# Kernel tuning notes

Measured on AMD Instinct MI355X. Metric: run time of the kernel, lower is better.

The kernel has to match this reference:

```python
import jax, jax.numpy as jnp
import numpy as np

B, S, H = 1, 2048, 2048
E, I = 16, 1408
I_SHARED = 5632
TOP_K = 2


def setup_inputs() -> dict:
    key = jax.random.key(0)
    ks = jax.random.split(key, 8)
    scale = 0.02
    return {
        "hidden_states": jax.random.normal(ks[0], (B, S, H), dtype=jnp.float32),
        "router_w": jax.random.normal(ks[1], (H, E), dtype=jnp.float32) * scale,
        "expert_gate_up_w": jax.random.normal(ks[2], (E, H, 2 * I), dtype=jnp.float32) * scale,
        "expert_out_w": jax.random.normal(ks[3], (E, I, H), dtype=jnp.float32) * scale,
        "shared_ffw_gate_w": jax.random.normal(ks[4], (H, I_SHARED), dtype=jnp.float32) * scale,
        "shared_ffw_inter_w": jax.random.normal(ks[5], (H, I_SHARED), dtype=jnp.float32) * scale,
        "shared_ffw_out_w": jax.random.normal(ks[6], (I_SHARED, H), dtype=jnp.float32) * scale,
        "shared_gate_w": jax.random.normal(ks[7], (H, 1), dtype=jnp.float32) * scale,
        "top_k": TOP_K,
    }


def reference(hidden_states, router_w, expert_gate_up_w, expert_out_w,
              shared_ffw_gate_w, shared_ffw_inter_w, shared_ffw_out_w,
              shared_gate_w, top_k):
    b, s, h = hidden_states.shape
    e = router_w.shape[-1]
    x = hidden_states.reshape(-1, h)  # [T, H]

    # --- Router: softmax over experts, top-k, renormalize (norm_top_k_prob=True) ---
    router_logits = x @ router_w                        # [T, E]
    router_probs = jax.nn.softmax(router_logits, -1)
    top_p, top_i = jax.lax.top_k(router_probs, top_k)   # [T, K]
    top_p = top_p / jnp.sum(top_p, axis=-1, keepdims=True)
    # dense routing matrix [E, T] (matches one_hot-sum-transpose in source)
    one_hot = jax.nn.one_hot(top_i, e, dtype=top_p.dtype)  # [T, K, E]
    routing_full = jnp.sum(one_hot * top_p[..., None], axis=1).T  # [E, T]

    # --- Dense per-expert SwiGLU over ALL tokens (as in QwenMoeExperts) ---
    gate_up = jnp.einsum('th,ehm->etm', x, expert_gate_up_w)  # [E, T, 2I]
    gate, up = jnp.split(gate_up, 2, axis=-1)
    hidden = up * jax.nn.silu(gate)                           # [E, T, I]
    expert_out = jnp.einsum('eti,eih->eth', hidden, expert_out_w)  # [E, T, H]
    expert_contribution = jnp.einsum('eth,et->th', expert_out, routing_full)

    # --- Shared expert (SwiGLU MLP) with sigmoid gate ---
    sgate = jax.nn.silu(x @ shared_ffw_gate_w)
    sinter = x @ shared_ffw_inter_w
    shared_out = (sinter * sgate) @ shared_ffw_out_w          # [T, H]
    shared_out = shared_out * jax.nn.sigmoid(x @ shared_gate_w)

    out = (expert_contribution + shared_out).reshape(b, s, h)
    return out, router_logits
```

## Files before the change

kernel.cpp:

```cpp
#include <hip/hip_runtime.h>
#include <math.h>

typedef __attribute__((ext_vector_type(4))) float f32x4;
typedef __attribute__((ext_vector_type(2))) unsigned int u32x2;
typedef __attribute__((ext_vector_type(4))) unsigned int u32x4;
typedef __attribute__((ext_vector_type(8))) unsigned short u16x8;
typedef __attribute__((ext_vector_type(8))) __bf16 bf16x8;
typedef unsigned short ushort_t;

#define H_DIM 2048
#define T_TOK 2048
#define NEXP 16
#define I_DIM 1408
#define I2_DIM 2816
#define IS_DIM 5632
#define MAXROWS 8192

static __device__ __forceinline__ unsigned short f2bf(float f){
  union { float f; unsigned u; } v; v.f = f;
  unsigned r = v.u + 0x7FFFu + ((v.u >> 16) & 1u);
  return (unsigned short)(r >> 16);
}
static __device__ __forceinline__ float bf2f(unsigned short h){
  union { unsigned u; float f; } v; v.u = ((unsigned)h) << 16;
  return v.f;
}
static __device__ __forceinline__ float silu_f(float x){ return x / (1.f + __expf(-x)); }

static __device__ __forceinline__ void gld16(const ushort_t* g, ushort_t* l){
  __builtin_amdgcn_global_load_lds(
      (const __attribute__((address_space(1))) unsigned int*)g,
      (__attribute__((address_space(3))) unsigned int*)l, 16, 0, 0);
}

__global__ void cast_bf16_k(const float* __restrict__ in, ushort_t* __restrict__ out){
  long i = ((long)blockIdx.x * 256 + threadIdx.x) * 8;
  f32x4 a = *(const f32x4*)&in[i];
  f32x4 b = *(const f32x4*)&in[i + 4];
  union { ushort_t s[8]; u32x4 v; } pk;
  #pragma unroll
  for (int j = 0; j < 4; j++){ pk.s[j] = f2bf(a[j]); pk.s[j+4] = f2bf(b[j]); }
  *(u32x4*)&out[i] = pk.v;
}

__global__ void transpose_cast_k(const float* __restrict__ in, ushort_t* __restrict__ out,
                                 int K, int N){
  long zo = (long)blockIdx.z * K * N;
  in += zo; out += zo;
  __shared__ float tl[64][65];
  int n0 = blockIdx.x * 64, k0 = blockIdx.y * 64;
  int tid = threadIdx.x;
  int lr = tid >> 2;
  int lv = (tid & 3) * 4;
  #pragma unroll
  for (int j = 0; j < 4; j++){
    int col = lv + j * 16;
    f32x4 v = *(const f32x4*)&in[(long)(k0 + lr) * N + n0 + col];
    tl[lr][col + 0] = v[0]; tl[lr][col + 1] = v[1];
    tl[lr][col + 2] = v[2]; tl[lr][col + 3] = v[3];
  }
  __syncthreads();
  int nl = tid >> 3;
  int kc = (tid & 7) * 8;
  #pragma unroll
  for (int it = 0; it < 2; it++){
    int n = nl + it * 32;
    union { ushort_t s[8]; u32x4 v; } pk;
    #pragma unroll
    for (int j = 0; j < 8; j++) pk.s[j] = f2bf(tl[kc + j][n]);
    *(u32x4*)&out[(long)(n0 + n) * K + k0 + kc] = pk.v;
  }
}

__global__ void router_k(const float* __restrict__ x, const float* __restrict__ rw,
                         const float* __restrict__ sgw, float* __restrict__ logits,
                         int* __restrict__ counts, int* __restrict__ lists,
                         float* __restrict__ probs, float* __restrict__ sgmul){
  int wid = threadIdx.x >> 6, lane = threadIdx.x & 63;
  int t = blockIdx.x * 4 + wid;
  const float* xr = x + (long)t * H_DIM;
  float acc[17];
  #pragma unroll
  for (int e = 0; e < 17; e++) acc[e] = 0.f;
  for (int h0 = lane * 4; h0 < H_DIM; h0 += 256){
    f32x4 xv = *(const f32x4*)&xr[h0];
    #pragma unroll
    for (int i = 0; i < 4; i++){
      float xs = xv[i];
      const float* wrow = rw + (long)(h0 + i) * NEXP;
      #pragma unroll
      for (int e = 0; e < 16; e++) acc[e] += xs * wrow[e];
      acc[16] += xs * sgw[h0 + i];
    }
  }
  #pragma unroll
  for (int e = 0; e < 17; e++)
    for (int off = 32; off >= 1; off >>= 1)
      acc[e] += __shfl_xor(acc[e], off);
  if (lane == 0){
    float* lo = logits + (long)t * NEXP;
    #pragma unroll
    for (int e = 0; e < 16; e++) lo[e] = acc[e];
    int e0 = 0;
    #pragma unroll
    for (int e = 1; e < 16; e++) if (acc[e] > acc[e0]) e0 = e;
    int e1 = (e0 == 0) ? 1 : 0;
    #pragma unroll
    for (int e = 0; e < 16; e++) if (e != e0 && acc[e] > acc[e1]) e1 = e;
    float d = acc[e1] - acc[e0];
    float ed = __expf(d);
    float p0 = 1.f / (1.f + ed);
    float p1 = ed / (1.f + ed);
    int pos0 = atomicAdd(&counts[e0], 1);
    lists[e0 * T_TOK + pos0] = t; probs[e0 * T_TOK + pos0] = p0;
    int pos1 = atomicAdd(&counts[e1], 1);
    lists[e1 * T_TOK + pos1] = t; probs[e1 * T_TOK + pos1] = p1;
    sgmul[t] = 1.f / (1.f + __expf(-acc[16]));
  }
}

__global__ void bases_k(const int* __restrict__ counts, int* __restrict__ bases){
  if (threadIdx.x == 0){
    int r = 0;
    for (int e = 0; e < NEXP; e++){ bases[e] = r; r += (counts[e] + 255) & ~255; }
  }
}

__global__ void swiglu_expert_k(const ushort_t* __restrict__ gu, ushort_t* __restrict__ hid){
  long qd = (long)blockIdx.x * 256 + threadIdx.x;
  long r = qd / (I_DIM / 8); int ic = (int)(qd % (I_DIM / 8)) * 8;
  const ushort_t* g = gu + r * I2_DIM + ic;
  u16x8 gv = *(const u16x8*)g;
  u16x8 uv = *(const u16x8*)(g + I_DIM);
  u16x8 ov;
  #pragma unroll
  for (int i = 0; i < 8; i++)
    ov[i] = f2bf(bf2f(uv[i]) * silu_f(bf2f(gv[i])));
  *(u16x8*)&hid[r * I_DIM + ic] = ov;
}

__global__ void swiglu_flat_k(ushort_t* __restrict__ sg, const ushort_t* __restrict__ si){
  long i = ((long)blockIdx.x * 256 + threadIdx.x) * 8;
  u16x8 g = *(const u16x8*)&sg[i];
  u16x8 s = *(const u16x8*)&si[i];
  u16x8 o;
  #pragma unroll
  for (int j = 0; j < 8; j++)
    o[j] = f2bf(bf2f(s[j]) * silu_f(bf2f(g[j])));
  *(u16x8*)&sg[i] = o;
}

template<int MODE>
__global__ __launch_bounds__(512, 2)
void gemm2_k(const ushort_t* __restrict__ A, const ushort_t* __restrict__ Bt,
             const ushort_t* __restrict__ Bt2, ushort_t* __restrict__ Cb,
             int K, int lda, int ldbt, int ldc, int mb,
             const int* __restrict__ counts, const int* __restrict__ bases,
             const int* __restrict__ lists, const float* __restrict__ probs,
             const float* __restrict__ svec, float* __restrict__ outp,
             long bstride){
  int z = blockIdx.z;
  int cnt = T_TOK;
  const ushort_t* Ab = A;
  const ushort_t* Bb = Bt;
  long rbase = 0;
  if constexpr (MODE == 0){ if (z){ Bb = Bt2; Cb += (long)T_TOK * ldc; } }
  if constexpr (MODE == 1){ cnt = counts[z]; rbase = bases[z]; Bb += (long)z * bstride; }
  if constexpr (MODE == 2){ cnt = counts[z]; Ab += (long)bases[z] * lda; Bb += (long)z * bstride; }

  int kb = K / gridDim.y;
  int kbase = blockIdx.y * kb;
  Ab += kbase;
  Bb += kbase;

  int nwg = gridDim.x;
  int wgo = blockIdx.x;
  int q = nwg >> 3, r = nwg & 7;
  int xcd = wgo & 7, idx = wgo >> 3;
  int wg = (xcd < r ? xcd * (q + 1) : r * (q + 1) + (xcd - r) * q) + idx;
  int m0 = (wg % mb) * 256;
  if (m0 >= cnt) return;
  int n0 = (wg / mb) * 128;

  extern __shared__ ushort_t lds[];

  int tid = threadIdx.x;
  int lane = tid & 63;
  int wv = tid >> 6;
  int wm = wv >> 1;
  int wn = wv & 1;

  int sg = ((lane & 7) ^ (lane >> 3)) * 8;
  long aoff0 = 0, boff0;
  long aoffg[4];
  {
    int r0 = lane >> 3;
    if constexpr (MODE == 1){
      #pragma unroll
      for (int j = 0; j < 4; j++){
        int jj = m0 + wv * 32 + j * 8 + r0; if (jj >= cnt) jj = cnt - 1;
        aoffg[j] = (long)lists[z * T_TOK + jj] * lda + sg;
      }
    } else {
      aoff0 = (long)(m0 + wv * 32 + r0) * lda + sg;
    }
    boff0 = (long)(n0 + wv * 16 + r0) * ldbt + sg;
  }

  auto stage = [&](int t, int buf){
    long ko = (long)t * 64;
    ushort_t* dA = lds + buf * 24576 + (wv * 32) * 64;
    ushort_t* dB = lds + buf * 24576 + 16384 + (wv * 16) * 64;
    #pragma unroll
    for (int j = 0; j < 4; j++){
      long ao;
      if constexpr (MODE == 1) ao = aoffg[j]; else ao = aoff0 + (long)(j * 8) * lda;
      gld16(Ab + ao + ko, dA + j * 512);
    }
    #pragma unroll
    for (int j = 0; j < 2; j++)
      gld16(Bb + boff0 + (long)(j * 8) * ldbt + ko, dB + j * 512);
  };

  f32x4 zero = {0.f, 0.f, 0.f, 0.f};
  f32x4 acc[4][4];
  #pragma unroll
  for (int i = 0; i < 4; i++)
    #pragma unroll
    for (int j = 0; j < 4; j++) acc[i][j] = zero;

  int nt = kb >> 6;
  stage(0, 0);
  __builtin_amdgcn_sched_barrier(0);
  stage(1, 1);

  int rb = 0, sb = 2;
  for (int t = 0; t < nt; t++){
    if (t + 1 < nt) asm volatile("s_waitcnt vmcnt(6)" ::: "memory");
    else            asm volatile("s_waitcnt vmcnt(0)" ::: "memory");
    __builtin_amdgcn_s_barrier();
    __builtin_amdgcn_sched_barrier(0);
    const ushort_t* tA = lds + rb * 24576;
    const ushort_t* tB = tA + 16384;
    bf16x8 af[2][4], bg[2][4];
    #pragma unroll
    for (int kk = 0; kk < 2; kk++){
      int cs = ((kk * 4 + (lane >> 4)) ^ (lane & 7)) * 8;
      #pragma unroll
      for (int f = 0; f < 4; f++){
        af[kk][f] = *(const bf16x8*)&tA[(wm*64 + f*16 + (lane & 15)) * 64 + cs];
        bg[kk][f] = *(const bf16x8*)&tB[(wn*64 + f*16 + (lane & 15)) * 64 + cs];
      }
    }
    __builtin_amdgcn_sched_barrier(0);
    if (t + 2 < nt) stage(t + 2, sb);
    #pragma unroll
    for (int kk = 0; kk < 2; kk++)
      #pragma unroll
      for (int fm = 0; fm < 4; fm++)
        #pragma unroll
        for (int fn = 0; fn < 4; fn++)
          acc[fm][fn] = __builtin_amdgcn_mfma_f32_16x16x32_bf16(af[kk][fm], bg[kk][fn], acc[fm][fn], 0, 0, 0);
    rb = (rb == 2) ? 0 : rb + 1;
    sb = (sb == 2) ? 0 : sb + 1;
  }

  int colb = n0 + wn * 64 + (lane & 15);
  int rowb = m0 + wm * 64 + (lane >> 4) * 4;
  #pragma unroll
  for (int fm = 0; fm < 4; fm++){
    #pragma unroll
    for (int fn = 0; fn < 4; fn++){
      f32x4 v = acc[fm][fn];
      int col = colb + fn * 16;
      #pragma unroll
      for (int rr = 0; rr < 4; rr++){
        int m = rowb + fm * 16 + rr;
        if constexpr (MODE == 0){
          Cb[(long)m * ldc + col] = f2bf(v[rr]);
        } else if constexpr (MODE == 1){
          if (m < cnt) Cb[(rbase + m) * (long)ldc + col] = f2bf(v[rr]);
        } else if constexpr (MODE == 2){
          if (m < cnt){
            int tok = lists[z * T_TOK + m];
            float pp = probs[z * T_TOK + m];
            atomicAdd(outp + (long)tok * ldc + col, pp * v[rr]);
          }
        } else {
          atomicAdd(outp + (long)m * ldc + col, svec[m] * v[rr]);
        }
      }
    }
  }
}

extern "C" void kernel_launch(void* const* d_in, const int* in_sizes, int n_in,
                              void* d_out, int out_size, void* d_ws, size_t ws_size,
                              hipStream_t stream){
  const float* x    = (const float*)d_in[0];
  const float* rw   = (const float*)d_in[1];
  const float* wgu  = (const float*)d_in[2];
  const float* wout = (const float*)d_in[3];
  const float* wsg  = (const float*)d_in[4];
  const float* wsi  = (const float*)d_in[5];
  const float* wso  = (const float*)d_in[6];
  const float* sgw  = (const float*)d_in[7];

  float* out = (float*)d_out;
  float* logits = out + (size_t)T_TOK * H_DIM;

  char* w = (char*)d_ws;
  auto alloc = [&](size_t b){ char* p = w; w += (b + 255) & ~(size_t)255; return p; };
  ushort_t* xb     = (ushort_t*)alloc((size_t)T_TOK * H_DIM * 2);
  ushort_t* wgu_t  = (ushort_t*)alloc((size_t)NEXP * I2_DIM * H_DIM * 2);
  ushort_t* wout_t = (ushort_t*)alloc((size_t)NEXP * H_DIM * I_DIM * 2);
  ushort_t* wsg_t  = (ushort_t*)alloc((size_t)IS_DIM * H_DIM * 2);
  ushort_t* wsi_t  = (ushort_t*)alloc((size_t)IS_DIM * H_DIM * 2);
  ushort_t* wso_t  = (ushort_t*)alloc((size_t)H_DIM * IS_DIM * 2);
  ushort_t* sgr    = (ushort_t*)alloc((size_t)2 * T_TOK * IS_DIM * 2);
  ushort_t* sir    = sgr + (size_t)T_TOK * IS_DIM;
  ushort_t* gu     = (ushort_t*)alloc((size_t)MAXROWS * I2_DIM * 2);
  ushort_t* hid    = (ushort_t*)alloc((size_t)MAXROWS * I_DIM * 2);
  int*   counts = (int*)alloc(64);
  int*   bases  = (int*)alloc(64);
  int*   lists  = (int*)alloc((size_t)NEXP * T_TOK * 4);
  float* probs  = (float*)alloc((size_t)NEXP * T_TOK * 4);
  float* sgmul  = (float*)alloc((size_t)T_TOK * 4);

  hipMemsetAsync(counts, 0, 64, stream);
  hipMemsetAsync(out, 0, (size_t)T_TOK * H_DIM * sizeof(float), stream);

  cast_bf16_k<<<2048, 256, 0, stream>>>(x, xb);
  transpose_cast_k<<<dim3(I2_DIM/64, H_DIM/64, NEXP), 256, 0, stream>>>(wgu, wgu_t, H_DIM, I2_DIM);
  transpose_cast_k<<<dim3(H_DIM/64, I_DIM/64, NEXP), 256, 0, stream>>>(wout, wout_t, I_DIM, H_DIM);
  transpose_cast_k<<<dim3(IS_DIM/64, H_DIM/64, 1), 256, 0, stream>>>(wsg, wsg_t, H_DIM, IS_DIM);
  transpose_cast_k<<<dim3(IS_DIM/64, H_DIM/64, 1), 256, 0, stream>>>(wsi, wsi_t, H_DIM, IS_DIM);
  transpose_cast_k<<<dim3(H_DIM/64, IS_DIM/64, 1), 256, 0, stream>>>(wso, wso_t, IS_DIM, H_DIM);

  router_k<<<512, 256, 0, stream>>>(x, rw, sgw, logits, counts, lists, probs, sgmul);
  bases_k<<<1, 64, 0, stream>>>(counts, bases);

  const size_t LDSB = 3 * 24576 * sizeof(ushort_t);

  gemm2_k<0><<<dim3((T_TOK/256) * (IS_DIM/128), 1, 2), 512, LDSB, stream>>>(
      xb, wsg_t, wsi_t, sgr, H_DIM, H_DIM, H_DIM, IS_DIM, T_TOK/256,
      nullptr, nullptr, nullptr, nullptr, nullptr, nullptr, 0);
  swiglu_flat_k<<<(T_TOK * (IS_DIM/8)) / 256, 256, 0, stream>>>(sgr, sir);
  gemm2_k<3><<<dim3((T_TOK/256) * (H_DIM/128), 4, 1), 512, LDSB, stream>>>(
      sgr, wso_t, nullptr, nullptr, IS_DIM, IS_DIM, IS_DIM, H_DIM, T_TOK/256,
      nullptr, nullptr, nullptr, nullptr, sgmul, out, 0);

  gemm2_k<1><<<dim3((T_TOK/256) * (I2_DIM/128), 1, NEXP), 512, LDSB, stream>>>(
      xb, wgu_t, nullptr, gu, H_DIM, H_DIM, H_DIM, I2_DIM, T_TOK/256,
      counts, bases, lists, probs, nullptr, nullptr, (long)I2_DIM * H_DIM);
  swiglu_expert_k<<<((long)MAXROWS * (I_DIM/8)) / 256, 256, 0, stream>>>(gu, hid);
  gemm2_k<2><<<dim3((T_TOK/256) * (H_DIM/128), 1, NEXP), 512, LDSB, stream>>>(
      hid, wout_t, nullptr, nullptr, I_DIM, I_DIM, I_DIM, H_DIM, T_TOK/256,
      counts, bases, lists, probs, nullptr, out, (long)I_DIM * H_DIM);

  (void)in_sizes; (void)n_in; (void)out_size; (void)ws_size;
}
```

Baseline: 848.6 us.

## Shrink GEMM tiles to 128x128 with 256 threads and K-step 32

Replaces the 256x128-tile, 512-thread GEMM with a 128x128-tile, 256-thread version using a K-step of 32, static LDS, a new swizzle and inline-asm ds_read_b128 loads. The GEMM bodies are split into separate kernels per mode, and expert row padding drops from 256 to 128 to match the smaller M tile. MFMA sections are wrapped in s_setprio to favour math issue. The aim is less padding waste on the grouped expert GEMMs and more resident workgroups; in exchange each tile reuses less data and the loop synchronises twice as often per K.

Result: faster. 798.9 us (-5.9%).

```diff
diff --git a/kernel.cpp b/kernel.cpp
--- a/kernel.cpp
+++ b/kernel.cpp
@@ -2,7 +2,6 @@
 #include <math.h>
 
 typedef __attribute__((ext_vector_type(4))) float f32x4;
-typedef __attribute__((ext_vector_type(2))) unsigned int u32x2;
 typedef __attribute__((ext_vector_type(4))) unsigned int u32x4;
 typedef __attribute__((ext_vector_type(8))) unsigned short u16x8;
 typedef __attribute__((ext_vector_type(8))) __bf16 bf16x8;
@@ -31,6 +30,12 @@
   __builtin_amdgcn_global_load_lds(
       (const __attribute__((address_space(1))) unsigned int*)g,
       (__attribute__((address_space(3))) unsigned int*)l, 16, 0, 0);
+}
+
+static __device__ __forceinline__ bf16x8 dsr128(unsigned byte_off){
+  u32x4 r;
+  asm volatile("ds_read_b128 %0, %1" : "=v"(r) : "v"(byte_off));
+  return __builtin_bit_cast(bf16x8, r);
 }
 
 __global__ void cast_bf16_k(const float* __restrict__ in, ushort_t* __restrict__ out){
@@ -122,7 +127,7 @@
 __global__ void bases_k(const int* __restrict__ counts, int* __restrict__ bases){
   if (threadIdx.x == 0){
     int r = 0;
-    for (int e = 0; e < NEXP; e++){ bases[e] = r; r += (counts[e] + 255) & ~255; }
+    for (int e = 0; e < NEXP; e++){ bases[e] = r; r += (counts[e] + 127) & ~127; }
   }
 }
 
@@ -151,14 +156,13 @@
 }
 
 template<int MODE>
-__global__ __launch_bounds__(512, 2)
-void gemm2_k(const ushort_t* __restrict__ A, const ushort_t* __restrict__ Bt,
-             const ushort_t* __restrict__ Bt2, ushort_t* __restrict__ Cb,
-             int K, int lda, int ldbt, int ldc, int mb,
-             const int* __restrict__ counts, const int* __restrict__ bases,
-             const int* __restrict__ lists, const float* __restrict__ probs,
-             const float* __restrict__ svec, float* __restrict__ outp,
-             long bstride){
+static __device__ __forceinline__ void gemm3_body(
+    const ushort_t* __restrict__ A, const ushort_t* __restrict__ Bt,
+    const ushort_t* __restrict__ Bt2, ushort_t* __restrict__ Cb,
+    int K, int lda, int ldbt, int ldc, int mb,
+    const int* __restrict__ counts, const int* __restrict__ bases,
+    const int* __restrict__ lists, const float* __restrict__ probs,
+    const float* __restrict__ svec, float* __restrict__ outp, long bstride){
   int z = blockIdx.z;
   int cnt = T_TOK;
   const ushort_t* Ab = A;
@@ -178,11 +182,12 @@
   int q = nwg >> 3, r = nwg & 7;
   int xcd = wgo & 7, idx = wgo >> 3;
   int wg = (xcd < r ? xcd * (q + 1) : r * (q + 1) + (xcd - r) * q) + idx;
-  int m0 = (wg % mb) * 256;
+  int m0 = (wg % mb) * 128;
   if (m0 >= cnt) return;
   int n0 = (wg / mb) * 128;
 
-  extern __shared__ ushort_t lds[];
+  __shared__ ushort_t lds[3 * 8192];
+  unsigned lbase = (unsigned)(size_t)(__attribute__((address_space(3))) ushort_t*)lds;
 
   int tid = threadIdx.x;
   int lane = tid & 63;
@@ -190,36 +195,31 @@
   int wm = wv >> 1;
   int wn = wv & 1;
 
-  int sg = ((lane & 7) ^ (lane >> 3)) * 8;
-  long aoff0 = 0, boff0;
-  long aoffg[4];
-  {
-    int r0 = lane >> 3;
+  int srow = lane >> 2;
+  int sslot = ((lane & 3) ^ (srow & 3)) * 8;
+  long aoff[2], boff[2];
+  #pragma unroll
+  for (int c = 0; c < 2; c++){
+    int mr = wv * 32 + c * 16 + srow;
+    int grow;
     if constexpr (MODE == 1){
-      #pragma unroll
-      for (int j = 0; j < 4; j++){
-        int jj = m0 + wv * 32 + j * 8 + r0; if (jj >= cnt) jj = cnt - 1;
-        aoffg[j] = (long)lists[z * T_TOK + jj] * lda + sg;
-      }
+      int j = m0 + mr; if (j >= cnt) j = cnt - 1;
+      grow = lists[z * T_TOK + j];
     } else {
-      aoff0 = (long)(m0 + wv * 32 + r0) * lda + sg;
+      grow = m0 + mr;
     }
-    boff0 = (long)(n0 + wv * 16 + r0) * ldbt + sg;
+    aoff[c] = (long)grow * lda + sslot;
+    boff[c] = (long)(n0 + mr) * ldbt + sslot;
   }
 
   auto stage = [&](int t, int buf){
-    long ko = (long)t * 64;
-    ushort_t* dA = lds + buf * 24576 + (wv * 32) * 64;
-    ushort_t* dB = lds + buf * 24576 + 16384 + (wv * 16) * 64;
-    #pragma unroll
-    for (int j = 0; j < 4; j++){
-      long ao;
-      if constexpr (MODE == 1) ao = aoffg[j]; else ao = aoff0 + (long)(j * 8) * lda;
-      gld16(Ab + ao + ko, dA + j * 512);
-    }
-    #pragma unroll
-    for (int j = 0; j < 2; j++)
-      gld16(Bb + boff0 + (long)(j * 8) * ldbt + ko, dB + j * 512);
+    long ko = (long)t * 32;
+    ushort_t* dA = lds + buf * 8192 + wv * 32 * 32;
+    ushort_t* dB = dA + 4096;
+    gld16(Ab + aoff[0] + ko, dA);
+    gld16(Ab + aoff[1] + ko, dA + 512);
+    gld16(Bb + boff[0] + ko, dB);
+    gld16(Bb + boff[1] + ko, dB + 512);
   };
 
   f32x4 zero = {0.f, 0.f, 0.f, 0.f};
@@ -229,38 +229,41 @@
     #pragma unroll
     for (int j = 0; j < 4; j++) acc[i][j] = zero;
 
-  int nt = kb >> 6;
+  int fr = lane & 15;
+  int kg = lane >> 4;
+  unsigned ps = (unsigned)((kg ^ (fr & 3)) << 4);
+  unsigned aoffb = (unsigned)((wm * 64 + fr) * 64) + ps;
+  unsigned boffb = 8192u + (unsigned)((wn * 64 + fr) * 64) + ps;
+
+  int nt = kb >> 5;
   stage(0, 0);
   __builtin_amdgcn_sched_barrier(0);
   stage(1, 1);
 
   int rb = 0, sb = 2;
   for (int t = 0; t < nt; t++){
-    if (t + 1 < nt) asm volatile("s_waitcnt vmcnt(6)" ::: "memory");
+    if (t + 2 < nt) asm volatile("s_waitcnt vmcnt(4)" ::: "memory");
     else            asm volatile("s_waitcnt vmcnt(0)" ::: "memory");
     __builtin_amdgcn_s_barrier();
     __builtin_amdgcn_sched_barrier(0);
-    const ushort_t* tA = lds + rb * 24576;
-    const ushort_t* tB = tA + 16384;
-    bf16x8 af[2][4], bg[2][4];
-    #pragma unroll
-    for (int kk = 0; kk < 2; kk++){
-      int cs = ((kk * 4 + (lane >> 4)) ^ (lane & 7)) * 8;
-      #pragma unroll
-      for (int f = 0; f < 4; f++){
-        af[kk][f] = *(const bf16x8*)&tA[(wm*64 + f*16 + (lane & 15)) * 64 + cs];
-        bg[kk][f] = *(const bf16x8*)&tB[(wn*64 + f*16 + (lane & 15)) * 64 + cs];
-      }
+    unsigned bufb = lbase + (unsigned)rb * 16384u;
+    bf16x8 af[4], bg[4];
+    #pragma unroll
+    for (int f = 0; f < 4; f++){
+      af[f] = dsr128(bufb + aoffb + f * 1024u);
+      bg[f] = dsr128(bufb + boffb + f * 1024u);
     }
     __builtin_amdgcn_sched_barrier(0);
     if (t + 2 < nt) stage(t + 2, sb);
-    #pragma unroll
-    for (int kk = 0; kk < 2; kk++)
+    asm volatile("s_waitcnt lgkmcnt(0)" ::: "memory");
+    __builtin_amdgcn_sched_barrier(0);
+    __builtin_amdgcn_s_setprio(1);
+    #pragma unroll
+    for (int fm = 0; fm < 4; fm++)
       #pragma unroll
-      for (int fm = 0; fm < 4; fm++)
-        #pragma unroll
-        for (int fn = 0; fn < 4; fn++)
-          acc[fm][fn] = __builtin_amdgcn_mfma_f32_16x16x32_bf16(af[kk][fm], bg[kk][fn], acc[fm][fn], 0, 0, 0);
+      for (int fn = 0; fn < 4; fn++)
+        acc[fm][fn] = __builtin_amdgcn_mfma_f32_16x16x32_bf16(af[fm], bg[fn], acc[fm][fn], 0, 0, 0);
+    __builtin_amdgcn_s_setprio(0);
     rb = (rb == 2) ? 0 : rb + 1;
     sb = (sb == 2) ? 0 : sb + 1;
   }
@@ -294,6 +297,16 @@
   }
 }
 
+#define GEMM_ARGS const ushort_t* A, const ushort_t* Bt, const ushort_t* Bt2, ushort_t* Cb, \
+    int K, int lda, int ldbt, int ldc, int mb, const int* counts, const int* bases, \
+    const int* lists, const float* probs, const float* svec, float* outp, long bstride
+#define GEMM_PASS A, Bt, Bt2, Cb, K, lda, ldbt, ldc, mb, counts, bases, lists, probs, svec, outp, bstride
+
+__global__ __launch_bounds__(256) void g_shared_gi(GEMM_ARGS){ gemm3_body<0>(GEMM_PASS); }
+__global__ __launch_bounds__(256) void g_shared_out(GEMM_ARGS){ gemm3_body<3>(GEMM_PASS); }
+__global__ __launch_bounds__(256) void g_expert_gu(GEMM_ARGS){ gemm3_body<1>(GEMM_PASS); }
+__global__ __launch_bounds__(256) void g_expert_out(GEMM_ARGS){ gemm3_body<2>(GEMM_PASS); }
+
 extern "C" void kernel_launch(void* const* d_in, const int* in_sizes, int n_in,
                               void* d_out, int out_size, void* d_ws, size_t ws_size,
                               hipStream_t stream){
@@ -340,22 +353,20 @@
   router_k<<<512, 256, 0, stream>>>(x, rw, sgw, logits, counts, lists, probs, sgmul);
   bases_k<<<1, 64, 0, stream>>>(counts, bases);
 
-  const size_t LDSB = 3 * 24576 * sizeof(ushort_t);
-
-  gemm2_k<0><<<dim3((T_TOK/256) * (IS_DIM/128), 1, 2), 512, LDSB, stream>>>(
-      xb, wsg_t, wsi_t, sgr, H_DIM, H_DIM, H_DIM, IS_DIM, T_TOK/256,
+  g_shared_gi<<<dim3((T_TOK/128) * (IS_DIM/128), 1, 2), 256, 0, stream>>>(
+      xb, wsg_t, wsi_t, sgr, H_DIM, H_DIM, H_DIM, IS_DIM, T_TOK/128,
       nullptr, nullptr, nullptr, nullptr, nullptr, nullptr, 0);
   swiglu_flat_k<<<(T_TOK * (IS_DIM/8)) / 256, 256, 0, stream>>>(sgr, sir);
-  gemm2_k<3><<<dim3((T_TOK/256) * (H_DIM/128), 4, 1), 512, LDSB, stream>>>(
-      sgr, wso_t, nullptr, nullptr, IS_DIM, IS_DIM, IS_DIM, H_DIM, T_TOK/256,
+  g_shared_out<<<dim3((T_TOK/128) * (H_DIM/128), 4, 1), 256, 0, stream>>>(
+      sgr, wso_t, nullptr, nullptr, IS_DIM, IS_DIM, IS_DIM, H_DIM, T_TOK/128,
       nullptr, nullptr, nullptr, nullptr, sgmul, out, 0);
 
-  gemm2_k<1><<<dim3((T_TOK/256) * (I2_DIM/128), 1, NEXP), 512, LDSB, stream>>>(
-      xb, wgu_t, nullptr, gu, H_DIM, H_DIM, H_DIM, I2_DIM, T_TOK/256,
+  g_expert_gu<<<dim3((T_TOK/128) * (I2_DIM/128), 1, NEXP), 256, 0, stream>>>(
+      xb, wgu_t, nullptr, gu, H_DIM, H_DIM, H_DIM, I2_DIM, T_TOK/128,
       counts, bases, lists, probs, nullptr, nullptr, (long)I2_DIM * H_DIM);
   swiglu_expert_k<<<((long)MAXROWS * (I_DIM/8)) / 256, 256, 0, stream>>>(gu, hid);
-  gemm2_k<2><<<dim3((T_TOK/256) * (H_DIM/128), 1, NEXP), 512, LDSB, stream>>>(
-      hid, wout_t, nullptr, nullptr, I_DIM, I_DIM, I_DIM, H_DIM, T_TOK/256,
+  g_expert_out<<<dim3((T_TOK/128) * (H_DIM/128), 1, NEXP), 256, 0, stream>>>(
+      hid, wout_t, nullptr, nullptr, I_DIM, I_DIM, I_DIM, H_DIM, T_TOK/128,
       counts, bases, lists, probs, nullptr, out, (long)I_DIM * H_DIM);
 
   (void)in_sizes; (void)n_in; (void)out_size; (void)ws_size;
```
